# Optimization experiments

Measured on AMD Instinct MI355X. Metric: run time of the kernel, lower is better.

## Reference

```python
import jax, jax.numpy as jnp
import numpy as np

B, T, N = 64, 100, 20000
ALPHA, BETA = 1.0, 0.5  # ExpRelu params


def setup_inputs() -> dict:
    rng = np.random.default_rng(0)
    # Proper SE(3) poses so the inverse is well-conditioned
    A = rng.normal(size=(B, 3, 3))
    Q, _ = np.linalg.qr(A)
    det = np.linalg.det(Q)
    Q[:, :, 0] *= det[:, None]  # force det(R) = +1
    poses = np.tile(np.eye(4, dtype=np.float64), (B, 1, 1))
    poses[:, :3, :3] = Q
    poses[:, :3, 3] = rng.normal(size=(B, 3)) * 10.0
    # Homogeneous global boundary points [4, N]
    pts = rng.normal(size=(3, N)) * 50.0
    boundary = np.concatenate([pts, np.ones((1, N))], axis=0)
    # Unit boundary normals [3, N]
    nrm = rng.normal(size=(3, N))
    nrm /= np.linalg.norm(nrm, axis=0, keepdims=True)
    # Local-frame waypoints [B, T, 3]
    wpts = rng.normal(size=(B, T, 3)) * 5.0
    return {
        "posesglobal": jnp.asarray(poses, dtype=jnp.float32),
        "waypointslocal": jnp.asarray(wpts, dtype=jnp.float32),
        "boundary": jnp.asarray(boundary, dtype=jnp.float32),
        "boundarynormals": jnp.asarray(nrm, dtype=jnp.float32),
    }


def _exp_relu(x):
    return jnp.where(x > 0.0, ALPHA * x + 1.0, jnp.exp(BETA * x))


def reference(posesglobal, waypointslocal, boundary, boundarynormals):
    posesinv = jnp.linalg.inv(posesglobal)                     # [B,4,4]
    # boundary points into each local frame: [B,N,3]
    bpl = jnp.einsum("bij,jn->bni", posesinv, boundary)[..., :3]
    # rotate normals into local frame: [B,N,3]
    bnl = jnp.einsum("bij,jn->bni", posesinv[:, :3, :3], boundarynormals)
    # 1-NN search: squared distances [B,T,N] (argmin-equivalent to cdist)
    w2 = jnp.sum(waypointslocal * waypointslocal, axis=-1)     # [B,T]
    p2 = jnp.sum(bpl * bpl, axis=-1)                           # [B,N]
    cross = jnp.einsum("btd,bnd->btn", waypointslocal, bpl)    # [B,T,N]
    d2 = w2[:, :, None] + p2[:, None, :] - 2.0 * cross
    idx = jnp.argmin(d2, axis=2)                               # [B,T]
    cp = jnp.take_along_axis(bpl, idx[..., None], axis=1)      # [B,T,3]
    cn = jnp.take_along_axis(bnl, idx[..., None], axis=1)      # [B,T,3]
    dots = jnp.sum((waypointslocal - cp) * cn, axis=2)         # [B,T]
    loss = jnp.mean(jnp.mean(_exp_relu(dots), axis=1))         # scalar
    return loss
```

## Files before the change

kernel.cpp:

```cpp
#include <hip/hip_runtime.h>
#include <math.h>
#include <float.h>

#define B_ 64
#define T_ 100
#define N_ 20000
#define NQ (B_ * T_)
#define NCHUNKS 250
#define CHUNK (N_ / NCHUNKS)
#define CPAIRS (CHUNK / 2)
#define GROUPS (CPAIRS / 2)
#define QG 640
#define NQG (NQ / QG)
#define QPT 10
#define K1_THREADS 64

typedef float f2 __attribute__((ext_vector_type(2)));
typedef float f4 __attribute__((ext_vector_type(4)));
typedef unsigned long long u64;

#define KEYS_OFF 0

__device__ __forceinline__ unsigned int f32_sortable(float f) {
    unsigned int u = __float_as_uint(f);
    return ((int)u >= 0) ? (u | 0x80000000u) : ~u;
}

__global__ __launch_bounds__(K1_THREADS) void k1_nn(
    const float* __restrict__ poses,
    const float* __restrict__ wpts,
    const float* __restrict__ boundary,
    u64* __restrict__ keys)
{
    __shared__ f4 sh[GROUPS][4];
    __shared__ float sposes[B_ * 16];

    const int bx   = blockIdx.x;
    const int qg   = bx / NCHUNKS;
    const int c    = bx - qg * NCHUNKS;
    const int base = c * CHUNK;
    const int tid  = threadIdx.x;

    {
        const f4* pg  = (const f4*)poses;
        f4*       sp4 = (f4*)sposes;
#pragma unroll
        for (int j = 0; j < 4; ++j)
            sp4[j * 64 + tid] = pg[j * 64 + tid];
    }

    if (tid < CPAIRS) {
        const int n0 = base + 2 * tid;
        const float x0 = boundary[n0],          x1 = boundary[n0 + 1];
        const float y0 = boundary[N_ + n0],     y1 = boundary[N_ + n0 + 1];
        const float z0 = boundary[2 * N_ + n0], z1 = boundary[2 * N_ + n0 + 1];
        f4 a = { -2.f * x0, -2.f * x1, -2.f * y0, -2.f * y1 };
        f4 b = { -2.f * z0, -2.f * z1,
                 x0 * x0 + y0 * y0 + z0 * z0,
                 x1 * x1 + y1 * y1 + z1 * z1 };
        sh[tid >> 1][(tid & 1) * 2 + 0] = a;
        sh[tid >> 1][(tid & 1) * 2 + 1] = b;
    }
    __syncthreads();

    float qx[QPT], qy[QPT], qz[QPT];
#pragma unroll
    for (int k = 0; k < QPT; ++k) {
        const int i = qg * QG + k * 64 + tid;
        const int b = i / T_;
        const float* P = sposes + b * 16;
        const float* W = wpts + i * 3;
        const float wx = W[0], wy = W[1], wz = W[2];
        qx[k] = P[0] * wx + P[1] * wy + P[2]  * wz + P[3];
        qy[k] = P[4] * wx + P[5] * wy + P[6]  * wz + P[7];
        qz[k] = P[8] * wx + P[9] * wy + P[10] * wz + P[11];
    }

    float beste[QPT];
    int   bg[QPT];
#pragma unroll
    for (int k = 0; k < QPT; ++k) { beste[k] = FLT_MAX; bg[k] = 0; }

#pragma unroll 4
    for (int g = 0; g < GROUPS; ++g) {
        const f4 A0 = sh[g][0], B0 = sh[g][1];
        const f4 A1 = sh[g][2], B1 = sh[g][3];
        const f2 mx0 = { A0.x, A0.y }, my0 = { A0.z, A0.w };
        const f2 mz0 = { B0.x, B0.y }, p20 = { B0.z, B0.w };
        const f2 mx1 = { A1.x, A1.y }, my1 = { A1.z, A1.w };
        const f2 mz1 = { B1.x, B1.y }, p21 = { B1.z, B1.w };

#pragma unroll
        for (int k = 0; k < QPT; ++k) {
            const f2 vx = { qx[k], qx[k] };
            const f2 vy = { qy[k], qy[k] };
            const f2 vz = { qz[k], qz[k] };
            f2 eA = __builtin_elementwise_fma(mx0, vx,
                    __builtin_elementwise_fma(my0, vy,
                    __builtin_elementwise_fma(mz0, vz, p20)));
            f2 eB = __builtin_elementwise_fma(mx1, vx,
                    __builtin_elementwise_fma(my1, vy,
                    __builtin_elementwise_fma(mz1, vz, p21)));
            f2 m2 = __builtin_elementwise_min(eA, eB);
            float m = fminf(m2.x, m2.y);
            const bool cc = m < beste[k];
            beste[k] = cc ? m : beste[k];
            bg[k]    = cc ? g : bg[k];
        }
    }

#pragma unroll
    for (int k = 0; k < QPT; ++k) {
        const int g = bg[k];
        const f4 A0 = sh[g][0], B0 = sh[g][1];
        const f4 A1 = sh[g][2], B1 = sh[g][3];
        const f2 mx0 = { A0.x, A0.y }, my0 = { A0.z, A0.w };
        const f2 mz0 = { B0.x, B0.y }, p20 = { B0.z, B0.w };
        const f2 mx1 = { A1.x, A1.y }, my1 = { A1.z, A1.w };
        const f2 mz1 = { B1.x, B1.y }, p21 = { B1.z, B1.w };
        const f2 vx = { qx[k], qx[k] };
        const f2 vy = { qy[k], qy[k] };
        const f2 vz = { qz[k], qz[k] };
        f2 eA = __builtin_elementwise_fma(mx0, vx,
                __builtin_elementwise_fma(my0, vy,
                __builtin_elementwise_fma(mz0, vz, p20)));
        f2 eB = __builtin_elementwise_fma(mx1, vx,
                __builtin_elementwise_fma(my1, vy,
                __builtin_elementwise_fma(mz1, vz, p21)));
        const int loc = base + 4 * g;
        const int li = (eA.x == beste[k]) ? loc
                     : (eA.y == beste[k]) ? loc + 1
                     : (eB.x == beste[k]) ? loc + 2 : loc + 3;
        const u64 key = ((u64)f32_sortable(beste[k]) << 32) | (unsigned)li;
        const int i = qg * QG + k * 64 + tid;
        atomicMin(&keys[i], key);
    }
}

__global__ __launch_bounds__(256) void k2_epilogue(
    const float* __restrict__ poses,
    const float* __restrict__ wpts,
    const float* __restrict__ boundary,
    const float* __restrict__ bnorm,
    const u64* __restrict__ keys,
    float* __restrict__ out)
{
    const int tid = threadIdx.x;
    const int i = blockIdx.x * 256 + tid;

    const int bi = (int)(unsigned)(keys[i] & 0xFFFFFFFFull);

    const int b = i / T_;
    const float* P = poses + b * 16;
    const float* W = wpts + i * 3;
    const float wx = W[0], wy = W[1], wz = W[2];
    const float qx = P[0] * wx + P[1] * wy + P[2]  * wz + P[3];
    const float qy = P[4] * wx + P[5] * wy + P[6]  * wz + P[7];
    const float qz = P[8] * wx + P[9] * wy + P[10] * wz + P[11];

    const float gx = boundary[bi], gy = boundary[N_ + bi], gz = boundary[2 * N_ + bi];
    const float nx = bnorm[bi],    ny = bnorm[N_ + bi],    nz = bnorm[2 * N_ + bi];

    const float dots = (qx - gx) * nx + (qy - gy) * ny + (qz - gz) * nz;
    float val = (dots > 0.0f) ? (dots + 1.0f) : expf(0.5f * dots);
    val *= (1.0f / (float)NQ);

    __shared__ float red[256];
    red[tid] = val;
    __syncthreads();
#pragma unroll
    for (int s = 128; s > 0; s >>= 1) {
        if (tid < s) red[tid] += red[tid + s];
        __syncthreads();
    }
    if (tid == 0) atomicAdd(out, red[0]);
}

extern "C" void kernel_launch(void* const* d_in, const int* in_sizes, int n_in,
                              void* d_out, int out_size, void* d_ws, size_t ws_size,
                              hipStream_t stream) {
    const float* poses    = (const float*)d_in[0];
    const float* wpts     = (const float*)d_in[1];
    const float* boundary = (const float*)d_in[2];
    const float* bnorm    = (const float*)d_in[3];
    float* out = (float*)d_out;

    u64* keys = (u64*)((char*)d_ws + KEYS_OFF);

    hipMemsetAsync(keys, 0xFF, NQ * sizeof(u64), stream);
    hipMemsetAsync(out, 0, sizeof(float), stream);

    k1_nn<<<NQG * NCHUNKS, K1_THREADS, 0, stream>>>(
        poses, wpts, boundary, keys);
    k2_epilogue<<<NQ / 256, 256, 0, stream>>>(
        poses, wpts, boundary, bnorm, keys, out);
}
```

Baseline: 85.87 us.

## Fuse NN search and epilogue via last-block ticket; track argmin index inline

Merges the nearest-neighbour kernel and the loss epilogue into one launch. Each block takes a ticket from an atomic counter, and the last block to finish computes the whole loss with a wave shuffle reduction. The argmin index is now tracked inside the hot loop instead of recomputing the winning group afterward. This removes a kernel launch and a memset, but adds per-candidate compare and select work in the inner loop. It also serialises the 6400-query epilogue onto a single 64-thread block.

```diff
diff --git a/kernel.cpp b/kernel.cpp
--- a/kernel.cpp
+++ b/kernel.cpp
@@ -13,27 +13,33 @@
 #define QG 640
 #define NQG (NQ / QG)
 #define QPT 10
-#define K1_THREADS 64
+#define NTHR 64
+#define NBLOCKS (NQG * NCHUNKS)
 
 typedef float f2 __attribute__((ext_vector_type(2)));
 typedef float f4 __attribute__((ext_vector_type(4)));
 typedef unsigned long long u64;
 
-#define KEYS_OFF 0
+#define KEYS_BYTES (NQ * sizeof(u64))
+#define CTR_OFF    KEYS_BYTES
 
 __device__ __forceinline__ unsigned int f32_sortable(float f) {
     unsigned int u = __float_as_uint(f);
     return ((int)u >= 0) ? (u | 0x80000000u) : ~u;
 }
 
-__global__ __launch_bounds__(K1_THREADS) void k1_nn(
+__global__ __launch_bounds__(NTHR) void k_fused(
     const float* __restrict__ poses,
     const float* __restrict__ wpts,
     const float* __restrict__ boundary,
-    u64* __restrict__ keys)
+    const float* __restrict__ bnorm,
+    u64* __restrict__ keys,
+    unsigned int* __restrict__ counter,
+    float* __restrict__ out)
 {
     __shared__ f4 sh[GROUPS][4];
     __shared__ float sposes[B_ * 16];
+    __shared__ unsigned int sticket;
 
     const int bx   = blockIdx.x;
     const int qg   = bx / NCHUNKS;
@@ -77,9 +83,9 @@
     }
 
     float beste[QPT];
-    int   bg[QPT];
+    int   bidx[QPT];
 #pragma unroll
-    for (int k = 0; k < QPT; ++k) { beste[k] = FLT_MAX; bg[k] = 0; }
+    for (int k = 0; k < QPT; ++k) { beste[k] = FLT_MAX; bidx[k] = 0; }
 
 #pragma unroll 4
     for (int g = 0; g < GROUPS; ++g) {
@@ -89,6 +95,7 @@
         const f2 mz0 = { B0.x, B0.y }, p20 = { B0.z, B0.w };
         const f2 mx1 = { A1.x, A1.y }, my1 = { A1.z, A1.w };
         const f2 mz1 = { B1.x, B1.y }, p21 = { B1.z, B1.w };
+        const int gbase = base + 4 * g;
 
 #pragma unroll
         for (int k = 0; k < QPT; ++k) {
@@ -103,77 +110,59 @@
                     __builtin_elementwise_fma(mz1, vz, p21)));
             f2 m2 = __builtin_elementwise_min(eA, eB);
             float m = fminf(m2.x, m2.y);
+            int slot = (m == eA.x) ? 0 : (m == eA.y) ? 1
+                     : (m == eB.x) ? 2 : 3;
             const bool cc = m < beste[k];
             beste[k] = cc ? m : beste[k];
-            bg[k]    = cc ? g : bg[k];
+            bidx[k]  = cc ? (gbase + slot) : bidx[k];
         }
     }
 
 #pragma unroll
     for (int k = 0; k < QPT; ++k) {
-        const int g = bg[k];
-        const f4 A0 = sh[g][0], B0 = sh[g][1];
-        const f4 A1 = sh[g][2], B1 = sh[g][3];
-        const f2 mx0 = { A0.x, A0.y }, my0 = { A0.z, A0.w };
-        const f2 mz0 = { B0.x, B0.y }, p20 = { B0.z, B0.w };
-        const f2 mx1 = { A1.x, A1.y }, my1 = { A1.z, A1.w };
-        const f2 mz1 = { B1.x, B1.y }, p21 = { B1.z, B1.w };
-        const f2 vx = { qx[k], qx[k] };
-        const f2 vy = { qy[k], qy[k] };
-        const f2 vz = { qz[k], qz[k] };
-        f2 eA = __builtin_elementwise_fma(mx0, vx,
-                __builtin_elementwise_fma(my0, vy,
-                __builtin_elementwise_fma(mz0, vz, p20)));
-        f2 eB = __builtin_elementwise_fma(mx1, vx,
-                __builtin_elementwise_fma(my1, vy,
-                __builtin_elementwise_fma(mz1, vz, p21)));
-        const int loc = base + 4 * g;
-        const int li = (eA.x == beste[k]) ? loc
-                     : (eA.y == beste[k]) ? loc + 1
-                     : (eB.x == beste[k]) ? loc + 2 : loc + 3;
-        const u64 key = ((u64)f32_sortable(beste[k]) << 32) | (unsigned)li;
-        const int i = qg * QG + k * 64 + tid;
-        atomicMin(&keys[i], key);
+        const u64 key = ((u64)f32_sortable(beste[k]) << 32)
+                      | (unsigned)bidx[k];
+        atomicMin(&keys[qg * QG + k * 64 + tid], key);
     }
-}
 
-__global__ __launch_bounds__(256) void k2_epilogue(
-    const float* __restrict__ poses,
-    const float* __restrict__ wpts,
-    const float* __restrict__ boundary,
-    const float* __restrict__ bnorm,
-    const u64* __restrict__ keys,
-    float* __restrict__ out)
-{
-    const int tid = threadIdx.x;
-    const int i = blockIdx.x * 256 + tid;
+    __syncthreads();
+    if (tid == 0) {
+        __threadfence();
+        sticket = atomicAdd(counter, 1u);
+    }
+    __syncthreads();
+    if (sticket != (unsigned)(NBLOCKS - 2)) return;
 
-    const int bi = (int)(unsigned)(keys[i] & 0xFFFFFFFFull);
+    __threadfence();
 
-    const int b = i / T_;
-    const float* P = poses + b * 16;
-    const float* W = wpts + i * 3;
-    const float wx = W[0], wy = W[1], wz = W[2];
-    const float qx = P[0] * wx + P[1] * wy + P[2]  * wz + P[3];
-    const float qy = P[4] * wx + P[5] * wy + P[6]  * wz + P[7];
-    const float qz = P[8] * wx + P[9] * wy + P[10] * wz + P[11];
+    float acc = 0.0f;
+    for (int i = tid; i < NQ; i += NTHR) {
+        const u64 key = __hip_atomic_load(&keys[i], __ATOMIC_RELAXED,
+                                          __HIP_MEMORY_SCOPE_AGENT);
+        const int bi = (int)(unsigned)(key & 0xFFFFFFFFull);
 
-    const float gx = boundary[bi], gy = boundary[N_ + bi], gz = boundary[2 * N_ + bi];
-    const float nx = bnorm[bi],    ny = bnorm[N_ + bi],    nz = bnorm[2 * N_ + bi];
+        const int b = i / T_;
+        const float* P = sposes + b * 16;
+        const float* W = wpts + i * 3;
+        const float wx = W[0], wy = W[1], wz = W[2];
+        const float qx2 = P[0] * wx + P[1] * wy + P[2]  * wz + P[3];
+        const float qy2 = P[4] * wx + P[5] * wy + P[6]  * wz + P[7];
+        const float qz2 = P[8] * wx + P[9] * wy + P[10] * wz + P[11];
 
-    const float dots = (qx - gx) * nx + (qy - gy) * ny + (qz - gz) * nz;
-    float val = (dots > 0.0f) ? (dots + 1.0f) : expf(0.5f * dots);
-    val *= (1.0f / (float)NQ);
+        const float gx = boundary[bi];
+        const float gy = boundary[N_ + bi];
+        const float gz = boundary[2 * N_ + bi];
+        const float nx = bnorm[bi];
+        const float ny = bnorm[N_ + bi];
+        const float nz = bnorm[2 * N_ + bi];
 
-    __shared__ float red[256];
-    red[tid] = val;
-    __syncthreads();
+        const float dots = (qx2 - gx) * nx + (qy2 - gy) * ny + (qz2 - gz) * nz;
+        acc += (dots > 0.0f) ? (dots + 1.0f) : expf(0.5f * dots);
+    }
 #pragma unroll
-    for (int s = 128; s > 0; s >>= 1) {
-        if (tid < s) red[tid] += red[tid + s];
-        __syncthreads();
-    }
-    if (tid == 0) atomicAdd(out, red[0]);
+    for (int off = 32; off > 0; off >>= 1)
+        acc += __shfl_down(acc, off, 64);
+    if (tid == 0) out[0] = acc * (1.0f / (float)NQ);
 }
 
 extern "C" void kernel_launch(void* const* d_in, const int* in_sizes, int n_in,
@@ -185,13 +174,11 @@
     const float* bnorm    = (const float*)d_in[3];
     float* out = (float*)d_out;
 
-    u64* keys = (u64*)((char*)d_ws + KEYS_OFF);
+    u64*          keys    = (u64*)d_ws;
+    unsigned int* counter = (unsigned int*)((char*)d_ws + CTR_OFF);
 
-    hipMemsetAsync(keys, 0xFF, NQ * sizeof(u64), stream);
-    hipMemsetAsync(out, 0, sizeof(float), stream);
+    hipMemsetAsync(d_ws, 0xFF, KEYS_BYTES + sizeof(unsigned int), stream);
 
-    k1_nn<<<NQG * NCHUNKS, K1_THREADS, 0, stream>>>(
-        poses, wpts, boundary, keys);
-    k2_epilogue<<<NQ / 256, 256, 0, stream>>>(
-        poses, wpts, boundary, bnorm, keys, out);
+    k_fused<<<NBLOCKS, NTHR, 0, stream>>>(
+        poses, wpts, boundary, bnorm, keys, counter, out);
 }
```

Result: slower. 205.2 us (+139.0%).

## Replace atomicMin merge with per-chunk partial keys and a separate reduction

Applied to the files above, without the earlier changes.

The NN kernel now writes each chunk's best key into a [chunks x queries] partial buffer instead of doing a global 64-bit atomicMin. The epilogue kernel scans all 250 partials per query, and a third kernel sums the block partials, so both memsets and the float atomicAdd go away. The best index is now tracked inside the hot loop rather than recomputed afterward, which adds compare and select work per iteration. The partial buffer costs about 12.8 MB of writes plus reads, and the k2 reduction loop over 250 chunks is serial per thread.

```diff
diff --git a/kernel.cpp b/kernel.cpp
--- a/kernel.cpp
+++ b/kernel.cpp
@@ -13,24 +13,27 @@
 #define QG 640
 #define NQG (NQ / QG)
 #define QPT 10
-#define K1_THREADS 64
+#define NTHR 64
+#define NBLOCKS (NQG * NCHUNKS)
+#define K2_BLOCKS (NQ / 256)
 
 typedef float f2 __attribute__((ext_vector_type(2)));
 typedef float f4 __attribute__((ext_vector_type(4)));
 typedef unsigned long long u64;
 
-#define KEYS_OFF 0
+#define PK_BYTES  ((size_t)NCHUNKS * NQ * sizeof(u64))
+#define BSUM_OFF  PK_BYTES
 
 __device__ __forceinline__ unsigned int f32_sortable(float f) {
     unsigned int u = __float_as_uint(f);
     return ((int)u >= 0) ? (u | 0x80000000u) : ~u;
 }
 
-__global__ __launch_bounds__(K1_THREADS) void k1_nn(
+__global__ __launch_bounds__(NTHR) void k1_nn(
     const float* __restrict__ poses,
     const float* __restrict__ wpts,
     const float* __restrict__ boundary,
-    u64* __restrict__ keys)
+    u64* __restrict__ pk)
 {
     __shared__ f4 sh[GROUPS][4];
     __shared__ float sposes[B_ * 16];
@@ -77,9 +80,9 @@
     }
 
     float beste[QPT];
-    int   bg[QPT];
+    int   bidx[QPT];
 #pragma unroll
-    for (int k = 0; k < QPT; ++k) { beste[k] = FLT_MAX; bg[k] = 0; }
+    for (int k = 0; k < QPT; ++k) { beste[k] = FLT_MAX; bidx[k] = 0; }
 
 #pragma unroll 4
     for (int g = 0; g < GROUPS; ++g) {
@@ -89,6 +92,7 @@
         const f2 mz0 = { B0.x, B0.y }, p20 = { B0.z, B0.w };
         const f2 mx1 = { A1.x, A1.y }, my1 = { A1.z, A1.w };
         const f2 mz1 = { B1.x, B1.y }, p21 = { B1.z, B1.w };
+        const int gbase = base + 4 * g;
 
 #pragma unroll
         for (int k = 0; k < QPT; ++k) {
@@ -103,52 +107,40 @@
                     __builtin_elementwise_fma(mz1, vz, p21)));
             f2 m2 = __builtin_elementwise_min(eA, eB);
             float m = fminf(m2.x, m2.y);
+            int slot = (m == eA.x) ? 0 : (m == eA.y) ? 1
+                     : (m == eB.x) ? 2 : 3;
             const bool cc = m < beste[k];
             beste[k] = cc ? m : beste[k];
-            bg[k]    = cc ? g : bg[k];
+            bidx[k]  = cc ? (gbase + slot) : bidx[k];
         }
     }
 
 #pragma unroll
     for (int k = 0; k < QPT; ++k) {
-        const int g = bg[k];
-        const f4 A0 = sh[g][0], B0 = sh[g][1];
-        const f4 A1 = sh[g][2], B1 = sh[g][3];
-        const f2 mx0 = { A0.x, A0.y }, my0 = { A0.z, A0.w };
-        const f2 mz0 = { B0.x, B0.y }, p20 = { B0.z, B0.w };
-        const f2 mx1 = { A1.x, A1.y }, my1 = { A1.z, A1.w };
-        const f2 mz1 = { B1.x, B1.y }, p21 = { B1.z, B1.w };
-        const f2 vx = { qx[k], qx[k] };
-        const f2 vy = { qy[k], qy[k] };
-        const f2 vz = { qz[k], qz[k] };
-        f2 eA = __builtin_elementwise_fma(mx0, vx,
-                __builtin_elementwise_fma(my0, vy,
-                __builtin_elementwise_fma(mz0, vz, p20)));
-        f2 eB = __builtin_elementwise_fma(mx1, vx,
-                __builtin_elementwise_fma(my1, vy,
-                __builtin_elementwise_fma(mz1, vz, p21)));
-        const int loc = base + 4 * g;
-        const int li = (eA.x == beste[k]) ? loc
-                     : (eA.y == beste[k]) ? loc + 1
-                     : (eB.x == beste[k]) ? loc + 2 : loc + 3;
-        const u64 key = ((u64)f32_sortable(beste[k]) << 32) | (unsigned)li;
-        const int i = qg * QG + k * 64 + tid;
-        atomicMin(&keys[i], key);
+        const u64 key = ((u64)f32_sortable(beste[k]) << 32)
+                      | (unsigned)bidx[k];
+        pk[(size_t)c * NQ + qg * QG + k * 64 + tid] = key;
     }
 }
 
-__global__ __launch_bounds__(256) void k2_epilogue(
+__global__ __launch_bounds__(256) void k2_reduce(
     const float* __restrict__ poses,
     const float* __restrict__ wpts,
     const float* __restrict__ boundary,
     const float* __restrict__ bnorm,
-    const u64* __restrict__ keys,
-    float* __restrict__ out)
+    const u64* __restrict__ pk,
+    float* __restrict__ bsum)
 {
     const int tid = threadIdx.x;
     const int i = blockIdx.x * 256 + tid;
 
-    const int bi = (int)(unsigned)(keys[i] & 0xFFFFFFFFull);
+    u64 best = pk[i];
+#pragma unroll 10
+    for (int c = 1; c < NCHUNKS; ++c) {
+        const u64 v = pk[(size_t)c * NQ + i];
+        best = (v < best) ? v : best;
+    }
+    const int bi = (int)(unsigned)(best & 0xFFFFFFFFull);
 
     const int b = i / T_;
     const float* P = poses + b * 16;
@@ -173,7 +165,19 @@
         if (tid < s) red[tid] += red[tid + s];
         __syncthreads();
     }
-    if (tid == 0) atomicAdd(out, red[0]);
+    if (tid == 0) bsum[blockIdx.x] = red[0];
+}
+
+__global__ __launch_bounds__(64) void k3_final(
+    const float* __restrict__ bsum,
+    float* __restrict__ out)
+{
+    const int tid = threadIdx.x;
+    float v = (tid < K2_BLOCKS) ? bsum[tid] : 0.0f;
+#pragma unroll
+    for (int off = 32; off > 0; off >>= 1)
+        v += __shfl_down(v, off, 64);
+    if (tid == 0) out[0] = v;
 }
 
 extern "C" void kernel_launch(void* const* d_in, const int* in_sizes, int n_in,
@@ -185,13 +189,11 @@
     const float* bnorm    = (const float*)d_in[3];
     float* out = (float*)d_out;
 
-    u64* keys = (u64*)((char*)d_ws + KEYS_OFF);
+    u64*   pk   = (u64*)d_ws;
+    float* bsum = (float*)((char*)d_ws + BSUM_OFF);
 
-    hipMemsetAsync(keys, 0xFF, NQ * sizeof(u64), stream);
-    hipMemsetAsync(out, 0, sizeof(float), stream);
-
-    k1_nn<<<NQG * NCHUNKS, K1_THREADS, 0, stream>>>(
-        poses, wpts, boundary, keys);
-    k2_epilogue<<<NQ / 256, 256, 0, stream>>>(
-        poses, wpts, boundary, bnorm, keys, out);
+    k1_nn<<<NBLOCKS, NTHR, 0, stream>>>(poses, wpts, boundary, pk);
+    k2_reduce<<<K2_BLOCKS, 256, 0, stream>>>(
+        poses, wpts, boundary, bnorm, pk, bsum);
+    k3_final<<<1, 64, 0, stream>>>(bsum, out);
 }
```

New measurement: 123.6 us. 1.44x slower.
